# Optimization experiments

Hardware: AMD Instinct MI355X
Metric: run time of the kernel (lower is better)

## Reference

```python
import jax, jax.numpy as jnp
import numpy as np

B, H, S, D = 2, 8, 2048, 64
N_HASHES = 6
EPS = 1e-8


def setup_inputs() -> dict:
    key = jax.random.key(0)
    kq, kk, kv, kr = jax.random.split(key, 4)
    Q = jax.random.normal(kq, (B, H, S, D), dtype=jnp.float32)
    K = jax.random.normal(kk, (B, H, S, D), dtype=jnp.float32)
    V = jax.random.normal(kv, (B, H, S, D), dtype=jnp.float32)
    rotations = jax.random.normal(kr, (H, N_HASHES, D), dtype=jnp.float32)
    return {"Q": Q, "K": K, "V": V, "rotations": rotations}


def _buckets(X, rotations, powers):
    # X: [b,h,l,d] -> integer bucket id per position, [b,h,l]
    Xn = X / (jnp.linalg.norm(X, axis=-1, keepdims=True) + 1e-8)
    bits = jnp.einsum('bhld,hnd->bhln', Xn, rotations) > 0
    return jnp.sum(bits.astype(jnp.int32) * powers, axis=-1)


def reference(Q, K, V, rotations):
    n_hashes = rotations.shape[1]
    d = Q.shape[-1]
    powers = (2 ** jnp.arange(n_hashes)).astype(jnp.int32)
    q_buckets = _buckets(Q, rotations, powers)  # [b,h,sq]
    k_buckets = _buckets(K, rotations, powers)  # [b,h,sk]
    # queries only attend to keys whose full hash code matches exactly
    match = q_buckets[..., :, None] == k_buckets[..., None, :]  # [b,h,sq,sk]
    scores = jnp.einsum('bhqd,bhkd->bhqk', Q, K) / (d ** 0.5)
    row_has = jnp.any(match, axis=-1, keepdims=True)
    masked = jnp.where(match, scores, -jnp.inf)
    m = jnp.max(masked, axis=-1, keepdims=True)
    m = jnp.where(row_has, m, 0.0)  # avoid -inf for empty rows
    e = jnp.where(match, jnp.exp(scores - m), 0.0)
    weights = e / (jnp.sum(e, axis=-1, keepdims=True) + EPS)
    out = jnp.einsum('bhqk,bhkd->bhqd', weights, V)
    return out / n_hashes
```

## Files before the change

### kernel.cpp

```cpp
#include <hip/hip_runtime.h>
#include <math.h>


constexpr int S_LEN = 2048;
constexpr int D = 64;
constexpr int NHASH = 6;
constexpr int BH = 16;
constexpr int NB = 64;
constexpr int QPAD = 4;
constexpr int PADQ = S_LEN + (QPAD - 1) * NB;
constexpr int NGRP = PADQ / QPAD;
constexpr int NBLK = NGRP / 4;
constexpr int KCH = 32;

__global__ __launch_bounds__(256) void lsh_buckets2(const float* __restrict__ Q,
                                                    const float* __restrict__ K,
                                                    const float* __restrict__ rot,
                                                    int* __restrict__ qb,
                                                    int* __restrict__ kb) {
    const int gw   = (blockIdx.x * 256 + threadIdx.x) >> 6;
    const int lane = threadIdx.x & 63;
    const bool isK = gw >= BH * S_LEN;
    const int wid  = isK ? gw - BH * S_LEN : gw;
    const float* X = isK ? K : Q;
    int* dst       = isK ? kb : qb;
    const int h    = (wid >> 11) & 7;

    const float x  = X[(size_t)wid * D + lane];
    const float* r = rot + (size_t)h * NHASH * D + lane;
    float p0 = x * r[0 * D], p1 = x * r[1 * D], p2 = x * r[2 * D];
    float p3 = x * r[3 * D], p4 = x * r[4 * D], p5 = x * r[5 * D];
#pragma unroll
    for (int off = 32; off >= 1; off >>= 1) {
        p0 += __shfl_xor(p0, off, 64);
        p1 += __shfl_xor(p1, off, 64);
        p2 += __shfl_xor(p2, off, 64);
        p3 += __shfl_xor(p3, off, 64);
        p4 += __shfl_xor(p4, off, 64);
        p5 += __shfl_xor(p5, off, 64);
    }
    int bucket = (p0 > 0.f ? 1 : 0) | (p1 > 0.f ? 2 : 0) | (p2 > 0.f ? 4 : 0) |
                 (p3 > 0.f ? 8 : 0) | (p4 > 0.f ? 16 : 0) | (p5 > 0.f ? 32 : 0);
    if (lane == 0) dst[wid] = bucket;
}

__global__ __launch_bounds__(256) void lsh_sortfuse(const int* __restrict__ qbuckets,
                                                    const int* __restrict__ kbuckets,
                                                    int* __restrict__ q_plist,
                                                    int* __restrict__ kstart_packed,
                                                    int* __restrict__ k_list) {
    __shared__ int hist[NB];
    __shared__ int start[NB];
    __shared__ int cur[NB];
    __shared__ int total;
    const int which = blockIdx.x >> 4;
    const int bh    = blockIdx.x & 15;
    const int tid   = threadIdx.x;
    const int* src  = (which ? kbuckets : qbuckets) + bh * S_LEN;

    if (tid < NB) hist[tid] = 0;
    __syncthreads();

    int myb[8];
#pragma unroll
    for (int i = 0; i < 8; ++i) {
        myb[i] = src[i * 256 + tid];
        atomicAdd(&hist[myb[i]], 1);
    }
    __syncthreads();

    if (tid < NB) {
        const int cnt = hist[tid];
        const int v   = which ? cnt : ((cnt + QPAD - 1) & ~(QPAD - 1));
        int x = v;
#pragma unroll
        for (int off = 1; off < 64; off <<= 1) {
            const int y = __shfl_up(x, off, 64);
            if (tid >= off) x += y;
        }
        const int st = x - v;
        start[tid] = st;
        cur[tid]   = st;
        if (which) kstart_packed[bh * NB + tid] = st | (cnt << 16);
        if (tid == 63) total = x;
    }
    __syncthreads();

    if (!which) {
        int* qp = q_plist + bh * PADQ;
        if (tid < NB) {
            const int cnt    = hist[tid];
            const int padded = (cnt + QPAD - 1) & ~(QPAD - 1);
            for (int t = start[tid] + cnt; t < start[tid] + padded; ++t) qp[t] = -1;
        }
        for (int t = total + tid; t < PADQ; t += 256) qp[t] = -1;
#pragma unroll
        for (int i = 0; i < 8; ++i) {
            const int b    = myb[i];
            const int slot = atomicAdd(&cur[b], 1);
            qp[slot] = (i * 256 + tid) | (b << 16);
        }
    } else {
        int* klp = k_list + bh * S_LEN;
#pragma unroll
        for (int i = 0; i < 8; ++i) {
            const int b    = myb[i];
            const int slot = atomicAdd(&cur[b], 1);
            klp[slot] = i * 256 + tid;
        }
    }
}

__global__ __launch_bounds__(256) void lsh_attn_d(const float* __restrict__ Q,
                                                  const float* __restrict__ K,
                                                  const float* __restrict__ V,
                                                  const int* __restrict__ q_plist,
                                                  const int* __restrict__ kstart_packed,
                                                  const int* __restrict__ k_list,
                                                  float* __restrict__ out) {
    __shared__ float qlds[4][QPAD][64];
    __shared__ float wbuf[4][QPAD][KCH];
    __shared__ int   kbuf[4][KCH];

    const int wv   = threadIdx.x >> 6;
    const int lane = threadIdx.x & 63;
    const int h    = lane >> 5;
    const int kk   = lane & 31;
    const int bh   = blockIdx.y;
    const int grp  = blockIdx.x * 4 + wv;

    const int* pl = q_plist + bh * PADQ + 4 * grp;
    const int e0 = __builtin_amdgcn_readfirstlane(pl[0]);
    if (e0 < 0) return;
    const int bucket = e0 >> 16;
    const int e1 = __builtin_amdgcn_readfirstlane(pl[1]);
    const int e2 = __builtin_amdgcn_readfirstlane(pl[2]);
    const int e3 = __builtin_amdgcn_readfirstlane(pl[3]);
    const int ksnk = __builtin_amdgcn_readfirstlane(kstart_packed[bh * NB + bucket]);
    const int ks = ksnk & 0xFFFF;
    const int nk = ksnk >> 16;

    const int q0 = e0 & 0xFFFF;
    const bool v1 = e1 >= 0, v2 = e2 >= 0, v3 = e3 >= 0;
    const int q1 = v1 ? (e1 & 0xFFFF) : q0;
    const int q2 = v2 ? (e2 & 0xFFFF) : q0;
    const int q3 = v3 ? (e3 & 0xFFFF) : q0;

    float* outb = out + (size_t)bh * S_LEN * D;
    if (nk == 0) {
        outb[(size_t)q0 * D + lane] = 0.0f;
        if (v1) outb[(size_t)q1 * D + lane] = 0.0f;
        if (v2) outb[(size_t)q2 * D + lane] = 0.0f;
        if (v3) outb[(size_t)q3 * D + lane] = 0.0f;
        return;
    }

    const int* kl   = k_list + bh * S_LEN + ks;
    const float* Kb = K + (size_t)bh * S_LEN * D;
    const float* Vb = V + (size_t)bh * S_LEN * D;
    const float* Qb = Q + (size_t)bh * S_LEN * D;

    qlds[wv][0][lane] = Qb[(size_t)q0 * D + lane];
    qlds[wv][1][lane] = Qb[(size_t)q1 * D + lane];
    qlds[wv][2][lane] = Qb[(size_t)q2 * D + lane];
    qlds[wv][3][lane] = Qb[(size_t)q3 * D + lane];

    float l0 = 0.f, l1 = 0.f;
    float acc[QPAD] = {0.f, 0.f, 0.f, 0.f};

    for (int c = 0; c * KCH < nk; ++c) {
        const int cnk  = min(KCH, nk - c * KCH);
        const int kidx = kl[c * KCH + min(kk, cnk - 1)];
        const float* krow = Kb + (size_t)kidx * D + h * 32;

        float4 kv[8];
#pragma unroll
        for (int i = 0; i < 8; ++i) kv[i] = *(const float4*)(krow + i * 4);

        float s[QPAD];
#pragma unroll
        for (int j = 0; j < QPAD; ++j) {
            const float* qj = &qlds[wv][j][h * 32];
            float sj = 0.f;
#pragma unroll
            for (int i = 0; i < 8; ++i) {
                const float4 qv = *(const float4*)(qj + i * 4);
                sj += qv.x * kv[i].x + qv.y * kv[i].y + qv.z * kv[i].z + qv.w * kv[i].w;
            }
            s[j] = sj;
        }
        s[0] += __shfl_xor(s[0], 32, 64);
        s[1] += __shfl_xor(s[1], 32, 64);
        s[2] += __shfl_xor(s[2], 32, 64);
        s[3] += __shfl_xor(s[3], 32, 64);

        const bool kvalid = kk < cnk;
        const float sa = h ? s[2] : s[0];
        const float sb = h ? s[3] : s[1];
        const float ea = kvalid ? __expf(sa * 0.125f) : 0.f;
        const float eb = kvalid ? __expf(sb * 0.125f) : 0.f;
        l0 += ea;
        l1 += eb;
        wbuf[wv][2 * h + 0][kk] = ea;
        wbuf[wv][2 * h + 1][kk] = eb;
        if (h == 0) kbuf[wv][kk] = kidx;

        const int ng = (cnk + 3) >> 2;
        for (int g = 0; g < ng; ++g) {
            const int4 kx = *(const int4*)&kbuf[wv][g * 4];
            const float vx = Vb[(size_t)kx.x * D + lane];
            const float vy = Vb[(size_t)kx.y * D + lane];
            const float vz = Vb[(size_t)kx.z * D + lane];
            const float vw = Vb[(size_t)kx.w * D + lane];
            const float4 eA = *(const float4*)&wbuf[wv][0][g * 4];
            const float4 eB = *(const float4*)&wbuf[wv][1][g * 4];
            const float4 eC = *(const float4*)&wbuf[wv][2][g * 4];
            const float4 eD = *(const float4*)&wbuf[wv][3][g * 4];
            acc[0] += eA.x * vx + eA.y * vy + eA.z * vz + eA.w * vw;
            acc[1] += eB.x * vx + eB.y * vy + eB.z * vz + eB.w * vw;
            acc[2] += eC.x * vx + eC.y * vy + eC.z * vz + eC.w * vw;
            acc[3] += eD.x * vx + eD.y * vy + eD.z * vz + eD.w * vw;
        }
    }

#pragma unroll
    for (int off = 16; off >= 1; off >>= 1) {
        l0 += __shfl_xor(l0, off, 64);
        l1 += __shfl_xor(l1, off, 64);
    }
    const float o0 = __shfl_xor(l0, 32, 64);
    const float o1 = __shfl_xor(l1, 32, 64);
    const float lq0 = h ? o0 : l0;
    const float lq1 = h ? o1 : l1;
    const float lq2 = h ? l0 : o0;
    const float lq3 = h ? l1 : o1;

    const float inv6 = 1.0f / 6.0f;
    outb[(size_t)q0 * D + lane] = acc[0] / (lq0 + 1e-8f) * inv6;
    if (v1) outb[(size_t)q1 * D + lane] = acc[1] / (lq1 + 1e-8f) * inv6;
    if (v2) outb[(size_t)q2 * D + lane] = acc[2] / (lq2 + 1e-8f) * inv6;
    if (v3) outb[(size_t)q3 * D + lane] = acc[3] / (lq3 + 1e-8f) * inv6;
}

extern "C" void kernel_launch(void* const* d_in, const int* in_sizes, int n_in,
                              void* d_out, int out_size, void* d_ws, size_t ws_size,
                              hipStream_t stream) {
    const float* Q   = (const float*)d_in[0];
    const float* K   = (const float*)d_in[1];
    const float* V   = (const float*)d_in[2];
    const float* rot = (const float*)d_in[3];
    float* out = (float*)d_out;

    char* ws = (char*)d_ws;
    int* q_buckets     = (int*)(ws);
    int* k_buckets     = (int*)(ws + 131072);
    int* k_list        = (int*)(ws + 262144);
    int* q_plist       = (int*)(ws + 393216);
    int* kstart_packed = (int*)(ws + 540672);

    lsh_buckets2<<<2 * BH * S_LEN / 4, 256, 0, stream>>>(Q, K, rot, q_buckets, k_buckets);
    lsh_sortfuse<<<32, 256, 0, stream>>>(q_buckets, k_buckets, q_plist, kstart_packed, k_list);
    lsh_attn_d<<<dim3(NBLK, BH), 256, 0, stream>>>(Q, K, V, q_plist, kstart_packed,
                                                   k_list, out);
}
```

Measured before the change: 73.46 us.

## Embed key-range metadata in padded query list and remap attention grid

The sort kernel now handles both Q and K buckets for each batch-head in a single block, running them one after the other, so it can write each bucket's key start and count straight into the query-group entries. This removes the separate kstart_packed table and the dependent second load in the attention kernel. The attention launch also becomes a 1-D grid with an interleaved bh mapping, which changes how work from different heads is spread across CUs. The cost is only 16 sort blocks instead of 32, each serialising the two sorts.

```diff
diff --git a/kernel.cpp b/kernel.cpp
--- a/kernel.cpp
+++ b/kernel.cpp
@@ -44,70 +44,92 @@
     if (lane == 0) dst[wid] = bucket;
 }
 
-__global__ __launch_bounds__(256) void lsh_sortfuse(const int* __restrict__ qbuckets,
-                                                    const int* __restrict__ kbuckets,
-                                                    int* __restrict__ q_plist,
-                                                    int* __restrict__ kstart_packed,
-                                                    int* __restrict__ k_list) {
+__global__ __launch_bounds__(256) void lsh_sortfuse_bh(const int* __restrict__ qbuckets,
+                                                       const int* __restrict__ kbuckets,
+                                                       int* __restrict__ q_plist,
+                                                       int* __restrict__ k_list) {
     __shared__ int hist[NB];
-    __shared__ int start[NB];
     __shared__ int cur[NB];
+    __shared__ int kst[NB], kcnt[NB];
+    __shared__ int qst[NB];
     __shared__ int total;
-    const int which = blockIdx.x >> 4;
-    const int bh    = blockIdx.x & 15;
-    const int tid   = threadIdx.x;
-    const int* src  = (which ? kbuckets : qbuckets) + bh * S_LEN;
+    const int bh  = blockIdx.x;
+    const int tid = threadIdx.x;
 
     if (tid < NB) hist[tid] = 0;
     __syncthreads();
-
-    int myb[8];
+    int myk[8];
 #pragma unroll
     for (int i = 0; i < 8; ++i) {
-        myb[i] = src[i * 256 + tid];
-        atomicAdd(&hist[myb[i]], 1);
-    }
-    __syncthreads();
-
+        myk[i] = kbuckets[bh * S_LEN + i * 256 + tid];
+        atomicAdd(&hist[myk[i]], 1);
+    }
+    __syncthreads();
     if (tid < NB) {
         const int cnt = hist[tid];
-        const int v   = which ? cnt : ((cnt + QPAD - 1) & ~(QPAD - 1));
-        int x = v;
+        int x = cnt;
 #pragma unroll
         for (int off = 1; off < 64; off <<= 1) {
             const int y = __shfl_up(x, off, 64);
             if (tid >= off) x += y;
         }
-        const int st = x - v;
-        start[tid] = st;
-        cur[tid]   = st;
-        if (which) kstart_packed[bh * NB + tid] = st | (cnt << 16);
-        if (tid == 63) total = x;
-    }
-    __syncthreads();
-
-    if (!which) {
-        int* qp = q_plist + bh * PADQ;
-        if (tid < NB) {
-            const int cnt    = hist[tid];
-            const int padded = (cnt + QPAD - 1) & ~(QPAD - 1);
-            for (int t = start[tid] + cnt; t < start[tid] + padded; ++t) qp[t] = -1;
-        }
-        for (int t = total + tid; t < PADQ; t += 256) qp[t] = -1;
+        kst[tid]  = x - cnt;
+        kcnt[tid] = cnt;
+        cur[tid]  = x - cnt;
+    }
+    __syncthreads();
+    {
+        int* klp = k_list + bh * S_LEN;
 #pragma unroll
         for (int i = 0; i < 8; ++i) {
-            const int b    = myb[i];
-            const int slot = atomicAdd(&cur[b], 1);
-            qp[slot] = (i * 256 + tid) | (b << 16);
-        }
-    } else {
-        int* klp = k_list + bh * S_LEN;
-#pragma unroll
-        for (int i = 0; i < 8; ++i) {
-            const int b    = myb[i];
+            const int b    = myk[i];
             const int slot = atomicAdd(&cur[b], 1);
             klp[slot] = i * 256 + tid;
         }
+    }
+    __syncthreads();
+
+    if (tid < NB) hist[tid] = 0;
+    __syncthreads();
+    int myq[8];
+#pragma unroll
+    for (int i = 0; i < 8; ++i) {
+        myq[i] = qbuckets[bh * S_LEN + i * 256 + tid];
+        atomicAdd(&hist[myq[i]], 1);
+    }
+    __syncthreads();
+    if (tid < NB) {
+        const int cnt = hist[tid];
+        const int v   = (cnt + QPAD - 1) & ~(QPAD - 1);
+        int x = v;
+#pragma unroll
+        for (int off = 1; off < 64; off <<= 1) {
+            const int y = __shfl_up(x, off, 64);
+            if (tid >= off) x += y;
+        }
+        qst[tid] = x - v;
+        cur[tid] = x - v;
+        if (tid == 63) total = x;
+    }
+    __syncthreads();
+
+    int* qp = q_plist + bh * PADQ;
+    if (tid < NB) {
+        const int cnt    = hist[tid];
+        const int padded = (cnt + QPAD - 1) & ~(QPAD - 1);
+        const int sent   = 0xFFFF | (kcnt[tid] << 16);
+        for (int t = qst[tid] + cnt; t < qst[tid] + padded; ++t) qp[t] = sent;
+    }
+    for (int t = total + tid; t < PADQ; t += 256) qp[t] = -1;
+#pragma unroll
+    for (int i = 0; i < 8; ++i) {
+        const int b    = myq[i];
+        const int slot = atomicAdd(&cur[b], 1);
+        const int pos  = slot & 3;
+        int e = i * 256 + tid;
+        if (pos == 0)      e |= kst[b] << 16;
+        else if (pos == 1) e |= kcnt[b] << 16;
+        qp[slot] = e;
     }
 }
 
@@ -115,7 +137,6 @@
                                                   const float* __restrict__ K,
                                                   const float* __restrict__ V,
                                                   const int* __restrict__ q_plist,
-                                                  const int* __restrict__ kstart_packed,
                                                   const int* __restrict__ k_list,
                                                   float* __restrict__ out) {
     __shared__ float qlds[4][QPAD][64];
@@ -126,25 +147,26 @@
     const int lane = threadIdx.x & 63;
     const int h    = lane >> 5;
     const int kk   = lane & 31;
-    const int bh   = blockIdx.y;
-    const int grp  = blockIdx.x * 4 + wv;
+    const int w    = blockIdx.x;
+    const int bh   = (w & 7) + 8 * ((w >> 3) & 1);
+    const int blk  = w >> 4;
+    const int grp  = blk * 4 + wv;
 
     const int* pl = q_plist + bh * PADQ + 4 * grp;
     const int e0 = __builtin_amdgcn_readfirstlane(pl[0]);
-    if (e0 < 0) return;
-    const int bucket = e0 >> 16;
+    if ((e0 & 0xFFFF) == 0xFFFF) return;
     const int e1 = __builtin_amdgcn_readfirstlane(pl[1]);
     const int e2 = __builtin_amdgcn_readfirstlane(pl[2]);
     const int e3 = __builtin_amdgcn_readfirstlane(pl[3]);
-    const int ksnk = __builtin_amdgcn_readfirstlane(kstart_packed[bh * NB + bucket]);
-    const int ks = ksnk & 0xFFFF;
-    const int nk = ksnk >> 16;
 
     const int q0 = e0 & 0xFFFF;
-    const bool v1 = e1 >= 0, v2 = e2 >= 0, v3 = e3 >= 0;
-    const int q1 = v1 ? (e1 & 0xFFFF) : q0;
-    const int q2 = v2 ? (e2 & 0xFFFF) : q0;
-    const int q3 = v3 ? (e3 & 0xFFFF) : q0;
+    const int ks = (unsigned)e0 >> 16;
+    const int nk = (unsigned)e1 >> 16;
+    const int t1 = e1 & 0xFFFF, t2 = e2 & 0xFFFF, t3 = e3 & 0xFFFF;
+    const bool v1 = t1 != 0xFFFF, v2 = t2 != 0xFFFF, v3 = t3 != 0xFFFF;
+    const int q1 = v1 ? t1 : q0;
+    const int q2 = v2 ? t2 : q0;
+    const int q3 = v3 ? t3 : q0;
 
     float* outb = out + (size_t)bh * S_LEN * D;
     if (nk == 0) {
@@ -252,14 +274,12 @@
     float* out = (float*)d_out;
 
     char* ws = (char*)d_ws;
-    int* q_buckets     = (int*)(ws);
-    int* k_buckets     = (int*)(ws + 131072);
-    int* k_list        = (int*)(ws + 262144);
-    int* q_plist       = (int*)(ws + 393216);
-    int* kstart_packed = (int*)(ws + 540672);
+    int* q_buckets = (int*)(ws);
+    int* k_buckets = (int*)(ws + 131072);
+    int* k_list    = (int*)(ws + 262144);
+    int* q_plist   = (int*)(ws + 393216);
 
     lsh_buckets2<<<2 * BH * S_LEN / 4, 256, 0, stream>>>(Q, K, rot, q_buckets, k_buckets);
-    lsh_sortfuse<<<32, 256, 0, stream>>>(q_buckets, k_buckets, q_plist, kstart_packed, k_list);
-    lsh_attn_d<<<dim3(NBLK, BH), 256, 0, stream>>>(Q, K, V, q_plist, kstart_packed,
-                                                   k_list, out);
-}
+    lsh_sortfuse_bh<<<BH, 256, 0, stream>>>(q_buckets, k_buckets, q_plist, k_list);
+    lsh_attn_d<<<NBLK * BH, 256, 0, stream>>>(Q, K, V, q_plist, k_list, out);
+}
```

Result: no change. 72.81 us (-0.9%).
